# Performance work log

Measured on AMD Instinct MI355X. Metric: run time of the kernel, lower is better.

The kernel has to match this reference:

```python
import jax, jax.numpy as jnp
import numpy as np

D_MODEL = 512
H = 8
DK = D_MODEL // H  # 64


def setup_inputs() -> dict:
    key = jax.random.key(0)
    ks = jax.random.split(key, 8)
    B, S = 2, 4096
    q = jax.random.normal(ks[0], (B, S, D_MODEL), dtype=jnp.float32)
    k = jax.random.normal(ks[1], (B, S, D_MODEL), dtype=jnp.float32)
    v = jax.random.normal(ks[2], (B, S, D_MODEL), dtype=jnp.float32)
    # per-head projection weights, torch nn.Linear layout [out, in], stacked over heads
    scale = 1.0 / np.sqrt(D_MODEL)
    Wq = jax.random.uniform(ks[3], (H, DK, D_MODEL), jnp.float32, -scale, scale)
    Wk = jax.random.uniform(ks[4], (H, DK, D_MODEL), jnp.float32, -scale, scale)
    Wv = jax.random.uniform(ks[5], (H, DK, D_MODEL), jnp.float32, -scale, scale)
    Wo = jax.random.uniform(ks[6], (D_MODEL, D_MODEL), jnp.float32, -scale, scale)
    # causal mask (True = keep), matches masked_fill(mask.logical_not(), -inf)
    mask = jnp.tril(jnp.ones((S, S), dtype=jnp.bool_))
    return {"q": q, "k": k, "v": v, "Wq": Wq, "Wk": Wk, "Wv": Wv, "Wo": Wo, "mask": mask}


def reference(q, k, v, Wq, Wk, Wv, Wo, mask):
    # per-head projections (stacked): x @ W^T for each head -> [B, H, S, DK]
    qh = jnp.einsum('bsd,hed->bhse', q, Wq)
    kh = jnp.einsum('bsd,hed->bhse', k, Wk)
    vh = jnp.einsum('bsd,hed->bhse', v, Wv)
    scaling = 1.0 / np.sqrt(DK)
    scores = jnp.einsum('bhse,bhte->bhst', qh, kh) * scaling  # [B,H,S,S]
    scores = jnp.where(mask, scores, -jnp.inf)
    attn = jax.nn.softmax(scores, axis=-1)
    heads = jnp.einsum('bhst,bhte->bhse', attn, vh)  # [B,H,S,DK]
    B, _, S, _ = heads.shape
    concat = jnp.transpose(heads, (0, 2, 1, 3)).reshape(B, S, D_MODEL)
    return concat @ Wo.T
```

## Files before the change

### kernel.cpp

```cpp
#include <hip/hip_runtime.h>
#include <hip/hip_bf16.h>
#include <math.h>

typedef __bf16 bf16_t;
typedef __bf16 bf16x8 __attribute__((ext_vector_type(8)));
typedef __bf16 bf16x4 __attribute__((ext_vector_type(4)));
typedef short short4v __attribute__((ext_vector_type(4)));
typedef float f32x4 __attribute__((ext_vector_type(4)));

__device__ __forceinline__ f32x4 mfma_k32(bf16x8 a, bf16x8 b, f32x4 c) {
    return __builtin_amdgcn_mfma_f32_16x16x32_bf16(a, b, c, 0, 0, 0);
}

__device__ __forceinline__ f32x4 mfma_k16(bf16x4 a, bf16x4 b, f32x4 c) {
#if __has_builtin(__builtin_amdgcn_mfma_f32_16x16x16_bf16)
    return __builtin_amdgcn_mfma_f32_16x16x16_bf16(a, b, c, 0, 0, 0);
#elif __has_builtin(__builtin_amdgcn_mfma_f32_16x16x16bf16_1k)
    short4v as, bs;
    __builtin_memcpy(&as, &a, 8);
    __builtin_memcpy(&bs, &b, 8);
    return __builtin_amdgcn_mfma_f32_16x16x16bf16_1k(as, bs, c, 0, 0, 0);
#else
    f32x4 d = c;
    asm volatile("v_mfma_f32_16x16x16_bf16 %0, %1, %2, %0" : "+v"(d) : "v"(a), "v"(b));
    return d;
#endif
}

__device__ __forceinline__ float fast_exp2(float x) {
#if __has_builtin(__builtin_amdgcn_exp2f)
    return __builtin_amdgcn_exp2f(x);
#else
    float r;
    asm("v_exp_f32 %0, %1" : "=v"(r) : "v"(x));
    return r;
#endif
}

__device__ __forceinline__ void async16(const bf16_t* g, __bf16* l) {
    __builtin_amdgcn_global_load_lds(
        (const __attribute__((address_space(1))) void*)g,
        (__attribute__((address_space(3))) void*)l, 16, 0, 0);
}

__device__ __forceinline__ int swz_col(int col, int row) {
    return (col & ~63) | ((((col >> 3) & 7) ^ (row & 7)) << 3) | (col & 7);
}

__global__ __launch_bounds__(256) void cvt_all(const float* __restrict__ q,
                                               const float* __restrict__ k,
                                               const float* __restrict__ v,
                                               const float* __restrict__ Wq,
                                               const float* __restrict__ Wk,
                                               const float* __restrict__ Wv,
                                               const float* __restrict__ Wo,
                                               bf16_t* __restrict__ qc,
                                               bf16_t* __restrict__ kc,
                                               bf16_t* __restrict__ vc,
                                               bf16_t* __restrict__ Wc) {
    const int bx = blockIdx.x;
    if (bx < 2048) {
        size_t i = ((size_t)bx * 256 + threadIdx.x) * 8;
        int row = (int)(i >> 9), col = (int)(i & 511);
        size_t di = (size_t)row * 512 + swz_col(col, row);
        float4 a0 = *(const float4*)(q + i), a1 = *(const float4*)(q + i + 4);
        float4 b0 = *(const float4*)(k + i), b1 = *(const float4*)(k + i + 4);
        float4 c0 = *(const float4*)(v + i), c1 = *(const float4*)(v + i + 4);
        bf16x8 qo, ko, vo;
        qo[0]=(__bf16)a0.x; qo[1]=(__bf16)a0.y; qo[2]=(__bf16)a0.z; qo[3]=(__bf16)a0.w;
        qo[4]=(__bf16)a1.x; qo[5]=(__bf16)a1.y; qo[6]=(__bf16)a1.z; qo[7]=(__bf16)a1.w;
        ko[0]=(__bf16)b0.x; ko[1]=(__bf16)b0.y; ko[2]=(__bf16)b0.z; ko[3]=(__bf16)b0.w;
        ko[4]=(__bf16)b1.x; ko[5]=(__bf16)b1.y; ko[6]=(__bf16)b1.z; ko[7]=(__bf16)b1.w;
        vo[0]=(__bf16)c0.x; vo[1]=(__bf16)c0.y; vo[2]=(__bf16)c0.z; vo[3]=(__bf16)c0.w;
        vo[4]=(__bf16)c1.x; vo[5]=(__bf16)c1.y; vo[6]=(__bf16)c1.z; vo[7]=(__bf16)c1.w;
        *(bf16x8*)(qc + di) = qo;
        *(bf16x8*)(kc + di) = ko;
        *(bf16x8*)(vc + di) = vo;
    } else {
        const int b2 = bx - 2048;
        const int m = b2 >> 7;
        const float* src = m == 0 ? Wq : m == 1 ? Wk : m == 2 ? Wv : Wo;
        const float sc = (m == 0) ? 0.125f * 1.44269504088896f : 1.0f;
        size_t i = ((size_t)(b2 & 127) * 256 + threadIdx.x) * 8;
        int row = (int)(i >> 9), col = (int)(i & 511);
        float4 a0 = *(const float4*)(src + i), a1 = *(const float4*)(src + i + 4);
        bf16x8 o;
        o[0]=(__bf16)(a0.x*sc); o[1]=(__bf16)(a0.y*sc); o[2]=(__bf16)(a0.z*sc); o[3]=(__bf16)(a0.w*sc);
        o[4]=(__bf16)(a1.x*sc); o[5]=(__bf16)(a1.y*sc); o[6]=(__bf16)(a1.z*sc); o[7]=(__bf16)(a1.w*sc);
        *(bf16x8*)(Wc + (size_t)m * 262144 + (size_t)row * 512 + swz_col(col, row)) = o;
    }
}

template<int MODE>
__device__ __forceinline__ void gemm128_body(const bf16_t* __restrict__ A,
                                             const bf16_t* __restrict__ B,
                                             void* __restrict__ outp,
                                             int m0, int n0) {
    __shared__ __bf16 Asm[128 * 64];
    __shared__ __bf16 Bsm[128 * 64];
    const int tid  = threadIdx.x;
    const int wave = tid >> 6;
    const int lane = tid & 63;
    const int quad = lane >> 4;
    const int l16  = lane & 15;
    const int swz  = l16 & 7;
    const int r8 = lane >> 3;
    const int c8 = (lane & 7) * 8;
    const int mrow0 = (wave & 1) * 64;
    const int ncol0 = (wave >> 1) * 64;

    f32x4 acc[4][4];
    for (int i = 0; i < 4; ++i)
        for (int j = 0; j < 4; ++j) acc[i][j] = (f32x4){0.f, 0.f, 0.f, 0.f};

    for (int kt = 0; kt < 512; kt += 64) {
        __syncthreads();
        for (int j = 0; j < 4; ++j) {
            async16(A + (size_t)(m0 + wave * 32 + j * 8 + r8) * 512 + kt + c8,
                    &Asm[(wave * 32 + j * 8) * 64]);
            async16(B + (size_t)(n0 + wave * 32 + j * 8 + r8) * 512 + kt + c8,
                    &Bsm[(wave * 32 + j * 8) * 64]);
        }
        __syncthreads();

        for (int ks = 0; ks < 2; ++ks) {
            bf16x8 af[4];
            for (int mt = 0; mt < 4; ++mt)
                af[mt] = *(const bf16x8*)&Asm[(mrow0 + mt * 16 + l16) * 64 + ((ks * 4 + quad) ^ swz) * 8];
            for (int nt = 0; nt < 4; ++nt) {
                bf16x8 bf = *(const bf16x8*)&Bsm[(ncol0 + nt * 16 + l16) * 64 + ((ks * 4 + quad) ^ swz) * 8];
                for (int mt = 0; mt < 4; ++mt)
                    acc[mt][nt] = mfma_k32(af[mt], bf, acc[mt][nt]);
            }
        }
    }

    if (MODE == 0) {
        bf16_t* out = (bf16_t*)outp;
        for (int nt = 0; nt < 4; ++nt) {
            int e = n0 + ncol0 + nt * 16 + l16;
            int h = e >> 6, el = e & 63;
            for (int mt = 0; mt < 4; ++mt)
                for (int r = 0; r < 4; ++r) {
                    int row = m0 + mrow0 + mt * 16 + quad * 4 + r;
                    int b = row >> 12, s = row & 4095;
                    int elp = (((el >> 3) ^ (row & 7)) << 3) | (el & 7);
                    out[(((size_t)(b * 8 + h)) * 4096 + s) * 64 + elp] = (bf16_t)acc[mt][nt][r];
                }
        }
    } else {
        bf16_t* out = (bf16_t*)outp;
        for (int nt = 0; nt < 4; ++nt) {
            int s_g = n0 + ncol0 + nt * 16 + l16;
            int b = s_g >> 12;
            int sbase = (s_g & 4095) & ~63;
            int f = 16 * ((l16 >> 2) & 3) + 4 * nt + (l16 & 3);
            for (int mt = 0; mt < 4; ++mt)
                for (int r = 0; r < 4; ++r) {
                    int e_g = m0 + mrow0 + mt * 16 + quad * 4 + r;
                    int h = e_g >> 6, el = e_g & 63;
                    int col = sbase | ((((f >> 3) ^ (e_g & 7)) & 7) << 3) | (f & 7);
                    out[(((size_t)(b * 8 + h)) * 64 + el) * 4096 + col] = (bf16_t)acc[mt][nt][r];
                }
        }
    }
}

__global__ __launch_bounds__(256) void proj_fused(const bf16_t* __restrict__ xs,
                                                  const bf16_t* __restrict__ Wc,
                                                  bf16_t* __restrict__ qh,
                                                  bf16_t* __restrict__ kh,
                                                  bf16_t* __restrict__ vh) {
    const int z = blockIdx.z;
    const bf16_t* X = xs + (size_t)z * 4194304;
    const bf16_t* W = Wc + (size_t)z * 262144;
    if (z == 0)
        gemm128_body<0>(X, W, qh, blockIdx.x * 128, blockIdx.y * 128);
    else if (z == 1)
        gemm128_body<0>(X, W, kh, blockIdx.x * 128, blockIdx.y * 128);
    else
        gemm128_body<1>(W, X, vh, blockIdx.y * 128, blockIdx.x * 128);
}

__global__ __launch_bounds__(256) void gemm_final(const bf16_t* __restrict__ Op,
                                                  const float* __restrict__ Lp,
                                                  const bf16_t* __restrict__ B,
                                                  float* __restrict__ out) {
    __shared__ __bf16 Asm[128 * 64];
    __shared__ __bf16 Bsm[128 * 64];
    const int m0 = blockIdx.x * 128, n0 = blockIdx.y * 128;
    const int tid  = threadIdx.x;
    const int wave = tid >> 6;
    const int lane = tid & 63;
    const int quad = lane >> 4;
    const int l16  = lane & 15;
    const int swz  = l16 & 7;
    const int r8 = lane >> 3;
    const int c8 = (lane & 7) * 8;
    const int mrow0 = (wave & 1) * 64;
    const int ncol0 = (wave >> 1) * 64;

    f32x4 acc[4][4];
    for (int i = 0; i < 4; ++i)
        for (int j = 0; j < 4; ++j) acc[i][j] = (f32x4){0.f, 0.f, 0.f, 0.f};

    for (int kt = 0; kt < 512; kt += 64) {
        const int h = kt >> 6;
        __syncthreads();
        for (int j = 0; j < 4; ++j)
            async16(B + (size_t)(n0 + wave * 32 + j * 8 + r8) * 512 + kt + c8,
                    &Bsm[(wave * 32 + j * 8) * 64]);
        for (int j = 0; j < 4; ++j) {
            const int rl  = wave * 32 + j * 8 + r8;
            const int row = m0 + rl;
            const int b   = row >> 12, sp = row & 4095;
            const size_t lidx = (size_t)(b * 8 + h) * 4096 + sp;
            bf16x8 a0 = *(const bf16x8*)(Op + lidx * 64 + c8);
            bf16x8 a1 = *(const bf16x8*)(Op + 4194304 + lidx * 64 + c8);
            float inv = 1.0f / (Lp[lidx] + Lp[65536 + lidx]);
            bf16x8 w;
            for (int i = 0; i < 8; ++i)
                w[i] = (bf16_t)(((float)a0[i] + (float)a1[i]) * inv);
            *(bf16x8*)&Asm[rl * 64 + (((lane & 7) ^ r8) << 3)] = w;
        }
        __syncthreads();

        for (int ks = 0; ks < 2; ++ks) {
            bf16x8 af[4];
            for (int mt = 0; mt < 4; ++mt)
                af[mt] = *(const bf16x8*)&Asm[(mrow0 + mt * 16 + l16) * 64 + ((ks * 4 + quad) ^ swz) * 8];
            for (int nt = 0; nt < 4; ++nt) {
                bf16x8 bf = *(const bf16x8*)&Bsm[(ncol0 + nt * 16 + l16) * 64 + ((ks * 4 + quad) ^ swz) * 8];
                for (int mt = 0; mt < 4; ++mt)
                    acc[mt][nt] = mfma_k32(af[mt], bf, acc[mt][nt]);
            }
        }
    }

    for (int nt = 0; nt < 4; ++nt) {
        int n = n0 + ncol0 + nt * 16 + l16;
        for (int mt = 0; mt < 4; ++mt)
            for (int r = 0; r < 4; ++r) {
                int row = m0 + mrow0 + mt * 16 + quad * 4 + r;
                out[(size_t)row * 512 + n] = acc[mt][nt][r];
            }
    }
}

__global__ __launch_bounds__(256, 4) void attn_kernel(const bf16_t* __restrict__ qh,
                                                      const bf16_t* __restrict__ kh,
                                                      const bf16_t* __restrict__ vh,
                                                      bf16_t* __restrict__ Opart,
                                                      float* __restrict__ Lpart) {
    __shared__ __bf16 SM[16384];
    __bf16* KSM = &SM[0];
    __bf16* VSM = &SM[8192];
    float* Osc = (float*)SM;
    float* Lsc = (float*)&SM[8320];

    const int id   = blockIdx.x;
    const int bh   = ((id & 7) << 1) | ((id >> 3) & 1);
    const int pair = (id >> 4) & 31;
    const int z    = (id >> 9) & 1;

    const int tid  = threadIdx.x;
    const int wave = tid >> 6;
    const int g2   = wave >> 1;
    const int wl   = wave & 1;
    const int lane = tid & 63;
    const int quad = lane >> 4;
    const int l16  = lane & 15;
    const int swz  = l16 & 7;
    const size_t base = (size_t)bh * 4096 * 64;
    const int r8 = lane >> 3;
    const int c8 = (lane & 7) * 8;

    bf16_t* Op = Opart + (size_t)z * 4194304;
    float*  Lp = Lpart + z * 65536;

    for (int leg = 0; leg < 2; ++leg) {
        const int qt = leg ? (63 - pair) : pair;
        const int q0 = qt * 64;

        bf16x8 qf[2][2];
        for (int g = 0; g < 2; ++g) {
            const bf16_t* qp = qh + base + (size_t)(q0 + wl * 32 + g * 16 + l16) * 64;
            qf[g][0] = *(const bf16x8*)(qp + ((quad ^ swz) * 8));
            qf[g][1] = *(const bf16x8*)(qp + (((4 + quad) ^ swz) * 8));
        }

        f32x4 o[2][4];
        for (int g = 0; g < 2; ++g)
            for (int i = 0; i < 4; ++i) o[g][i] = (f32x4){0.f, 0.f, 0.f, 0.f};
        float lsum[2] = {0.f, 0.f};

        const int S  = (qt + 2) >> 1;
        const int Sh = (S + 1) >> 1;
        const int it0 = z ? Sh : 0;
        const int it1 = z ? S : Sh;

        for (int it = it0; it < it1; ++it) {
            const int j0 = it * 128;
            __syncthreads();
            for (int p = 0; p < 2; ++p)
                for (int j = 0; j < 2; ++j) {
                    int row = wave * 16 + j * 8 + r8;
                    async16(kh + base + (size_t)(j0 + p * 64 + row) * 64 + c8,
                            KSM + (p * 64 + wave * 16 + j * 8) * 64);
                    async16(vh + (size_t)(bh * 64 + row) * 4096 + j0 + p * 64 + c8,
                            VSM + (p * 64 + wave * 16 + j * 8) * 64);
                }
            __syncthreads();

            const int pp = g2;
            const int koff = j0 + pp * 64 - q0;
            if (koff > wl * 32 + 31) continue;

            f32x4 st[2][4];
            for (int nt = 0; nt < 4; ++nt) {
                const __bf16* kr = KSM + (pp * 64 + nt * 16 + l16) * 64;
                bf16x8 kf0 = *(const bf16x8*)(kr + ((quad ^ swz) * 8));
                bf16x8 kf1 = *(const bf16x8*)(kr + (((4 + quad) ^ swz) * 8));
                for (int g = 0; g < 2; ++g) {
                    f32x4 zz = (f32x4){0.f, 0.f, 0.f, 0.f};
                    zz = mfma_k32(kf0, qf[g][0], zz);
                    zz = mfma_k32(kf1, qf[g][1], zz);
                    st[g][nt] = zz;
                }
            }

            bf16x4 pf[2][4];
            for (int g = 0; g < 2; ++g) {
                const int qb = wl * 32 + g * 16;
                if (koff + 63 <= qb) {
                    for (int nt = 0; nt < 4; ++nt)
                        for (int r = 0; r < 4; ++r) {
                            float p = fast_exp2(st[g][nt][r]);
                            lsum[g] += p;
                            pf[g][nt][r] = (bf16_t)p;
                        }
                } else {
                    const int qrow = qb + l16;
                    for (int nt = 0; nt < 4; ++nt)
                        for (int r = 0; r < 4; ++r) {
                            int key = nt * 16 + quad * 4 + r;
                            float p = (key + koff <= qrow) ? fast_exp2(st[g][nt][r]) : 0.f;
                            lsum[g] += p;
                            pf[g][nt][r] = (bf16_t)p;
                        }
                }
            }

            for (int dt = 0; dt < 4; ++dt)
                for (int kt2 = 0; kt2 < 2; ++kt2) {
                    bf16x8 vf = *(const bf16x8*)&VSM[(pp * 64 + dt * 16 + l16) * 64 + (((2 * quad + kt2) ^ swz) * 8)];
                    bf16x4 vlo = {vf[0], vf[1], vf[2], vf[3]};
                    bf16x4 vhi = {vf[4], vf[5], vf[6], vf[7]};
                    for (int g = 0; g < 2; ++g) {
                        o[g][dt] = mfma_k16(pf[g][2 * kt2], vlo, o[g][dt]);
                        o[g][dt] = mfma_k16(pf[g][2 * kt2 + 1], vhi, o[g][dt]);
                    }
                }
        }

        __syncthreads();
        if (g2 == 1) {
            for (int g = 0; g < 2; ++g) {
                float ls = lsum[g];
                ls += __shfl_xor(ls, 16);
                ls += __shfl_xor(ls, 32);
                const int qb = wl * 32 + g * 16;
                Lsc[qb + l16] = ls;
                for (int dt = 0; dt < 4; ++dt)
                    for (int r = 0; r < 4; ++r)
                        Osc[(qb + quad * 4 + r) * 65 + dt * 16 + l16] = o[g][dt][r];
            }
        }
        __syncthreads();
        if (g2 == 0) {
            for (int g = 0; g < 2; ++g) {
                float ls = lsum[g];
                ls += __shfl_xor(ls, 16);
                ls += __shfl_xor(ls, 32);
                const int qb = wl * 32 + g * 16;
                ls += Lsc[qb + l16];
                Lsc[qb + l16] = ls;
                for (int dt = 0; dt < 4; ++dt)
                    for (int r = 0; r < 4; ++r) {
                        int idx = (qb + quad * 4 + r) * 65 + dt * 16 + l16;
                        Osc[idx] = o[g][dt][r] + Osc[idx];
                    }
            }
        }
        __syncthreads();
        {
            const int q  = tid >> 2;
            const int e0 = (tid & 3) * 16;
            bf16x8 w0, w1;
            for (int i = 0; i < 8; ++i) {
                w0[i] = (bf16_t)Osc[q * 65 + e0 + i];
                w1[i] = (bf16_t)Osc[q * 65 + e0 + 8 + i];
            }
            size_t slot = ((size_t)(bh * 64 + qt)) * 4096 + q * 64 + e0;
            *(bf16x8*)&Op[slot]     = w0;
            *(bf16x8*)&Op[slot + 8] = w1;
            if (tid < 64) Lp[(bh * 64 + qt) * 64 + tid] = Lsc[tid];
        }
    }
}

extern "C" void kernel_launch(void* const* d_in, const int* in_sizes, int n_in,
                              void* d_out, int out_size, void* d_ws, size_t ws_size,
                              hipStream_t stream) {
    const float* q  = (const float*)d_in[0];
    const float* k  = (const float*)d_in[1];
    const float* v  = (const float*)d_in[2];
    const float* Wq = (const float*)d_in[3];
    const float* Wk = (const float*)d_in[4];
    const float* Wv = (const float*)d_in[5];
    const float* Wo = (const float*)d_in[6];
    float* out = (float*)d_out;

    bf16_t* ws = (bf16_t*)d_ws;
    const size_t R = (size_t)8192 * 512;
    bf16_t* qc = ws;
    bf16_t* kc = ws + R;
    bf16_t* vc = ws + 2 * R;
    bf16_t* vh = ws + 3 * R;
    bf16_t* Wc = ws + 4 * R;
    float*  Lp = (float*)(ws + 4 * R + 1048576);
    bf16_t* qh = (bf16_t*)d_out;
    bf16_t* kh = (bf16_t*)d_out + R;

    cvt_all<<<dim3(2560), dim3(256), 0, stream>>>(q, k, v, Wq, Wk, Wv, Wo, qc, kc, vc, Wc);
    proj_fused<<<dim3(64, 4, 3), dim3(256), 0, stream>>>(ws, Wc, qh, kh, vh);
    attn_kernel<<<dim3(1024), dim3(256), 0, stream>>>(qh, kh, vh, kc, Lp);
    gemm_final<<<dim3(64, 4), dim3(256), 0, stream>>>(kc, Lp, Wc + 3 * 262144, out);
}
```

Before: 239.4 us.

## Fuse fp32-to-bf16 activation conversion into projection GEMM loads, remap block order

Removes the separate pass that converted q/k/v to bf16 and wrote swizzled copies to workspace. The projection GEMM now loads fp32 activations directly, converts them in registers and stores swizzled bf16 into LDS, while weights are still converted by a small kernel. Block indices for the projection and final GEMMs are remapped so that groups of blocks share the same M tiles across N, which should improve L2 reuse. The cost is synchronous fp32 loads in place of async global-to-LDS copies, and double the bytes read from global memory per activation tile.

```diff
diff --git a/kernel.cpp b/kernel.cpp
--- a/kernel.cpp
+++ b/kernel.cpp
@@ -47,53 +47,36 @@
     return (col & ~63) | ((((col >> 3) & 7) ^ (row & 7)) << 3) | (col & 7);
 }
 
-__global__ __launch_bounds__(256) void cvt_all(const float* __restrict__ q,
-                                               const float* __restrict__ k,
-                                               const float* __restrict__ v,
-                                               const float* __restrict__ Wq,
-                                               const float* __restrict__ Wk,
-                                               const float* __restrict__ Wv,
-                                               const float* __restrict__ Wo,
-                                               bf16_t* __restrict__ qc,
-                                               bf16_t* __restrict__ kc,
-                                               bf16_t* __restrict__ vc,
-                                               bf16_t* __restrict__ Wc) {
-    const int bx = blockIdx.x;
-    if (bx < 2048) {
-        size_t i = ((size_t)bx * 256 + threadIdx.x) * 8;
-        int row = (int)(i >> 9), col = (int)(i & 511);
-        size_t di = (size_t)row * 512 + swz_col(col, row);
-        float4 a0 = *(const float4*)(q + i), a1 = *(const float4*)(q + i + 4);
-        float4 b0 = *(const float4*)(k + i), b1 = *(const float4*)(k + i + 4);
-        float4 c0 = *(const float4*)(v + i), c1 = *(const float4*)(v + i + 4);
-        bf16x8 qo, ko, vo;
-        qo[0]=(__bf16)a0.x; qo[1]=(__bf16)a0.y; qo[2]=(__bf16)a0.z; qo[3]=(__bf16)a0.w;
-        qo[4]=(__bf16)a1.x; qo[5]=(__bf16)a1.y; qo[6]=(__bf16)a1.z; qo[7]=(__bf16)a1.w;
-        ko[0]=(__bf16)b0.x; ko[1]=(__bf16)b0.y; ko[2]=(__bf16)b0.z; ko[3]=(__bf16)b0.w;
-        ko[4]=(__bf16)b1.x; ko[5]=(__bf16)b1.y; ko[6]=(__bf16)b1.z; ko[7]=(__bf16)b1.w;
-        vo[0]=(__bf16)c0.x; vo[1]=(__bf16)c0.y; vo[2]=(__bf16)c0.z; vo[3]=(__bf16)c0.w;
-        vo[4]=(__bf16)c1.x; vo[5]=(__bf16)c1.y; vo[6]=(__bf16)c1.z; vo[7]=(__bf16)c1.w;
-        *(bf16x8*)(qc + di) = qo;
-        *(bf16x8*)(kc + di) = ko;
-        *(bf16x8*)(vc + di) = vo;
-    } else {
-        const int b2 = bx - 2048;
-        const int m = b2 >> 7;
-        const float* src = m == 0 ? Wq : m == 1 ? Wk : m == 2 ? Wv : Wo;
-        const float sc = (m == 0) ? 0.125f * 1.44269504088896f : 1.0f;
-        size_t i = ((size_t)(b2 & 127) * 256 + threadIdx.x) * 8;
-        int row = (int)(i >> 9), col = (int)(i & 511);
-        float4 a0 = *(const float4*)(src + i), a1 = *(const float4*)(src + i + 4);
-        bf16x8 o;
-        o[0]=(__bf16)(a0.x*sc); o[1]=(__bf16)(a0.y*sc); o[2]=(__bf16)(a0.z*sc); o[3]=(__bf16)(a0.w*sc);
-        o[4]=(__bf16)(a1.x*sc); o[5]=(__bf16)(a1.y*sc); o[6]=(__bf16)(a1.z*sc); o[7]=(__bf16)(a1.w*sc);
-        *(bf16x8*)(Wc + (size_t)m * 262144 + (size_t)row * 512 + swz_col(col, row)) = o;
-    }
-}
-
-template<int MODE>
-__device__ __forceinline__ void gemm128_body(const bf16_t* __restrict__ A,
-                                             const bf16_t* __restrict__ B,
+__device__ __forceinline__ bf16x8 cvt8(float4 a, float4 b) {
+    bf16x8 w;
+    w[0]=(__bf16)a.x; w[1]=(__bf16)a.y; w[2]=(__bf16)a.z; w[3]=(__bf16)a.w;
+    w[4]=(__bf16)b.x; w[5]=(__bf16)b.y; w[6]=(__bf16)b.z; w[7]=(__bf16)b.w;
+    return w;
+}
+
+__global__ __launch_bounds__(256) void cvt_W(const float* __restrict__ Wq,
+                                             const float* __restrict__ Wk,
+                                             const float* __restrict__ Wv,
+                                             const float* __restrict__ Wo,
+                                             bf16_t* __restrict__ Wc) {
+    const int b2 = blockIdx.x;
+    const int m = b2 >> 7;
+    const float* src = m == 0 ? Wq : m == 1 ? Wk : m == 2 ? Wv : Wo;
+    const float sc = (m == 0) ? 0.125f * 1.44269504088896f : 1.0f;
+    size_t i = ((size_t)(b2 & 127) * 256 + threadIdx.x) * 8;
+    int row = (int)(i >> 9), col = (int)(i & 511);
+    float4 a0 = *(const float4*)(src + i), a1 = *(const float4*)(src + i + 4);
+    bf16x8 o;
+    o[0]=(__bf16)(a0.x*sc); o[1]=(__bf16)(a0.y*sc); o[2]=(__bf16)(a0.z*sc); o[3]=(__bf16)(a0.w*sc);
+    o[4]=(__bf16)(a1.x*sc); o[5]=(__bf16)(a1.y*sc); o[6]=(__bf16)(a1.z*sc); o[7]=(__bf16)(a1.w*sc);
+    *(bf16x8*)(Wc + (size_t)m * 262144 + (size_t)row * 512 + swz_col(col, row)) = o;
+}
+
+template<int MODE, int AF32, int BF32>
+__device__ __forceinline__ void gemm128_body(const bf16_t* __restrict__ Ab,
+                                             const float* __restrict__ Af,
+                                             const bf16_t* __restrict__ Bb,
+                                             const float* __restrict__ Bf,
                                              void* __restrict__ outp,
                                              int m0, int n0) {
     __shared__ __bf16 Asm[128 * 64];
@@ -116,10 +99,23 @@
     for (int kt = 0; kt < 512; kt += 64) {
         __syncthreads();
         for (int j = 0; j < 4; ++j) {
-            async16(A + (size_t)(m0 + wave * 32 + j * 8 + r8) * 512 + kt + c8,
-                    &Asm[(wave * 32 + j * 8) * 64]);
-            async16(B + (size_t)(n0 + wave * 32 + j * 8 + r8) * 512 + kt + c8,
-                    &Bsm[(wave * 32 + j * 8) * 64]);
+            const int rl = wave * 32 + j * 8 + r8;
+            if (AF32) {
+                const float* s = Af + (size_t)(m0 + rl) * 512 + kt + c8;
+                float4 v0 = *(const float4*)s, v1 = *(const float4*)(s + 4);
+                *(bf16x8*)&Asm[rl * 64 + (((lane & 7) ^ r8) << 3)] = cvt8(v0, v1);
+            } else {
+                async16(Ab + (size_t)(m0 + rl) * 512 + kt + c8,
+                        &Asm[(wave * 32 + j * 8) * 64]);
+            }
+            if (BF32) {
+                const float* s = Bf + (size_t)(n0 + rl) * 512 + kt + c8;
+                float4 v0 = *(const float4*)s, v1 = *(const float4*)(s + 4);
+                *(bf16x8*)&Bsm[rl * 64 + (((lane & 7) ^ r8) << 3)] = cvt8(v0, v1);
+            } else {
+                async16(Bb + (size_t)(n0 + rl) * 512 + kt + c8,
+                        &Bsm[(wave * 32 + j * 8) * 64]);
+            }
         }
         __syncthreads();
 
@@ -166,20 +162,24 @@
     }
 }
 
-__global__ __launch_bounds__(256) void proj_fused(const bf16_t* __restrict__ xs,
+__global__ __launch_bounds__(256) void proj_fused(const float* __restrict__ q,
+                                                  const float* __restrict__ k,
+                                                  const float* __restrict__ v,
                                                   const bf16_t* __restrict__ Wc,
                                                   bf16_t* __restrict__ qh,
                                                   bf16_t* __restrict__ kh,
                                                   bf16_t* __restrict__ vh) {
+    const int f = blockIdx.x;
+    const int y = (f >> 3) & 3;
+    const int x = (f & 7) | ((f >> 5) << 3);
     const int z = blockIdx.z;
-    const bf16_t* X = xs + (size_t)z * 4194304;
     const bf16_t* W = Wc + (size_t)z * 262144;
     if (z == 0)
-        gemm128_body<0>(X, W, qh, blockIdx.x * 128, blockIdx.y * 128);
+        gemm128_body<0, 1, 0>(nullptr, q, W, nullptr, qh, x * 128, y * 128);
     else if (z == 1)
-        gemm128_body<0>(X, W, kh, blockIdx.x * 128, blockIdx.y * 128);
+        gemm128_body<0, 1, 0>(nullptr, k, W, nullptr, kh, x * 128, y * 128);
     else
-        gemm128_body<1>(W, X, vh, blockIdx.y * 128, blockIdx.x * 128);
+        gemm128_body<1, 0, 1>(W, nullptr, nullptr, v, vh, y * 128, x * 128);
 }
 
 __global__ __launch_bounds__(256) void gemm_final(const bf16_t* __restrict__ Op,
@@ -188,7 +188,9 @@
                                                   float* __restrict__ out) {
     __shared__ __bf16 Asm[128 * 64];
     __shared__ __bf16 Bsm[128 * 64];
-    const int m0 = blockIdx.x * 128, n0 = blockIdx.y * 128;
+    const int fb = blockIdx.x;
+    const int m0 = ((fb & 7) | ((fb >> 5) << 3)) * 128;
+    const int n0 = ((fb >> 3) & 3) * 128;
     const int tid  = threadIdx.x;
     const int wave = tid >> 6;
     const int lane = tid & 63;
@@ -423,17 +425,15 @@
 
     bf16_t* ws = (bf16_t*)d_ws;
     const size_t R = (size_t)8192 * 512;
-    bf16_t* qc = ws;
-    bf16_t* kc = ws + R;
-    bf16_t* vc = ws + 2 * R;
+    bf16_t* opart = ws + R;
     bf16_t* vh = ws + 3 * R;
     bf16_t* Wc = ws + 4 * R;
     float*  Lp = (float*)(ws + 4 * R + 1048576);
     bf16_t* qh = (bf16_t*)d_out;
     bf16_t* kh = (bf16_t*)d_out + R;
 
-    cvt_all<<<dim3(2560), dim3(256), 0, stream>>>(q, k, v, Wq, Wk, Wv, Wo, qc, kc, vc, Wc);
-    proj_fused<<<dim3(64, 4, 3), dim3(256), 0, stream>>>(ws, Wc, qh, kh, vh);
-    attn_kernel<<<dim3(1024), dim3(256), 0, stream>>>(qh, kh, vh, kc, Lp);
-    gemm_final<<<dim3(64, 4), dim3(256), 0, stream>>>(kc, Lp, Wc + 3 * 262144, out);
-}
+    cvt_W<<<dim3(512), dim3(256), 0, stream>>>(Wq, Wk, Wv, Wo, Wc);
+    proj_fused<<<dim3(256, 1, 3), dim3(256), 0, stream>>>(q, k, v, Wc, qh, kh, vh);
+    attn_kernel<<<dim3(1024), dim3(256), 0, stream>>>(qh, kh, vh, opart, Lp);
+    gemm_final<<<dim3(256), dim3(256), 0, stream>>>(opart, Lp, Wc + 3 * 262144, out);
+}
```

After: 239.2 us. Within noise of the previous version (-0.1%).
